# Kernel optimization log

Hardware: AMD Instinct MI355X
Metric: run time of the kernel (lower is better)

## Reference

```python
import jax, jax.numpy as jnp
import numpy as np

DIM, HEADS, KV_HEADS = 1024, 16, 4
B, T = 1, 4096
HEAD_DIM = DIM // HEADS           # 64
KV_DIM = DIM // (HEADS // KV_HEADS)  # 256
SCALE = HEAD_DIM ** -0.5


def setup_inputs() -> dict:
    key = jax.random.key(0)
    ks = jax.random.split(key, 9)
    s = lambda fan_in: fan_in ** -0.5
    return {
        "x": jax.random.normal(ks[0], (B, T, DIM), jnp.float32),
        "mask": jnp.tril(jnp.ones((1, 1, T, T), jnp.bool_)),  # causal
        "q_w": jax.random.normal(ks[1], (DIM, DIM), jnp.float32) * s(DIM),
        "q_b": jnp.zeros((DIM,), jnp.float32),
        "k_w": jax.random.normal(ks[2], (KV_DIM, DIM), jnp.float32) * s(DIM),
        "k_b": jnp.zeros((KV_DIM,), jnp.float32),
        "v_w": jax.random.normal(ks[3], (KV_DIM, DIM), jnp.float32) * s(DIM),
        "v_b": jnp.zeros((KV_DIM,), jnp.float32),
        "o_w": jax.random.normal(ks[4], (DIM, DIM), jnp.float32) * s(DIM),
        "o_b": jnp.zeros((DIM,), jnp.float32),
    }


def reference(x, mask, q_w, q_b, k_w, k_b, v_w, v_b, o_w, o_b):
    b, t, d = x.shape
    g = HEADS // KV_HEADS  # query heads per kv head
    # projections (torch Linear: x @ W^T + b)
    q = (x @ q_w.T + q_b).reshape(b, t, HEADS, HEAD_DIM).transpose(0, 2, 1, 3)      # [B,H,T,hd]
    k = (x @ k_w.T + k_b).reshape(b, t, KV_HEADS, HEAD_DIM).transpose(0, 2, 1, 3)   # [B,Hk,T,hd]
    v = (x @ v_w.T + v_b).reshape(b, t, KV_HEADS, HEAD_DIM).transpose(0, 2, 1, 3)   # [B,Hk,T,hd]
    # GQA: group query heads over shared kv heads
    qg = q.reshape(b, KV_HEADS, g, t, HEAD_DIM)                                     # [B,Hk,g,T,hd]
    scores = jnp.einsum('bkgtd,bksd->bkgts', qg, k) * SCALE                         # [B,Hk,g,T,T]
    scores = jnp.where(mask[:, :, None, :, :], scores, -1e9)
    attn = jax.nn.softmax(scores, axis=-1)  # dropout is identity in eval mode
    out = jnp.einsum('bkgts,bksd->bkgtd', attn, v)                                  # [B,Hk,g,T,hd]
    out = out.reshape(b, HEADS, t, HEAD_DIM).transpose(0, 2, 1, 3).reshape(b, t, d)
    out = out @ o_w.T + o_b
    return out, k, v  # (output, new kv cache)
```

## Files before the change

kernel.cpp:

```cpp
#include <hip/hip_runtime.h>
#include <hip/hip_bf16.h>
#include <stdint.h>

typedef __bf16 bf16;
typedef __bf16 bf16x8 __attribute__((ext_vector_type(8)));
typedef float  f32x4 __attribute__((ext_vector_type(4)));

#define SEQ   4096
#define DIM_  1024
#define HD_   64
#define NEG_BIG (-30000.0f)

__device__ __forceinline__ bf16x8 cvt8(const float* p) {
    f32x4 a = *(const f32x4*)p, b = *(const f32x4*)(p + 4);
    bf16x8 r;
    r[0]=(bf16)a[0]; r[1]=(bf16)a[1]; r[2]=(bf16)a[2]; r[3]=(bf16)a[3];
    r[4]=(bf16)b[0]; r[5]=(bf16)b[1]; r[6]=(bf16)b[2]; r[7]=(bf16)b[3];
    return r;
}

template<int MODE>
__global__ __launch_bounds__(256)
void gemm_bt(const void* __restrict__ Av,
             const float* __restrict__ B0, const float* __restrict__ b0,
             const float* __restrict__ B1, const float* __restrict__ b1,
             const float* __restrict__ B2, const float* __restrict__ b2,
             float* __restrict__ C0, float* __restrict__ C1, float* __restrict__ C2,
             bf16* __restrict__ Qbf, bf16* __restrict__ Kbf, bf16* __restrict__ VTbf)
{
    const int K = 1024;
    const int tid  = threadIdx.x;
    const int lane = tid & 63, wave = tid >> 6;
    const int qd = lane >> 4, ln = lane & 15;
    const int wm = (wave & 1) * 32, wn = (wave >> 1) * 64;
    const int m0 = blockIdx.x * 64, n0 = blockIdx.y * 128;

    const float* Bp; const float* bias;
    if (MODE == 1) {
        if (n0 < 1024)      { Bp = B0 + (size_t)n0 * K;        bias = b0 + n0; }
        else if (n0 < 1280) { Bp = B1 + (size_t)(n0-1024) * K; bias = b1 + (n0-1024); }
        else                { Bp = B2 + (size_t)(n0-1280) * K; bias = b2 + (n0-1280); }
    } else                  { Bp = B0 + (size_t)n0 * K;        bias = b0 + n0; }

    __shared__ bf16 As[64*32];
    __shared__ bf16 Bs[128*32];

    f32x4 acc[2][4] = {};

    for (int k0 = 0; k0 < K; k0 += 32) {
        bf16x8 ra, rb[2];
        {
            int row = tid >> 2, ch = tid & 3;
            if (MODE == 0)
                ra = *(const bf16x8*)((const bf16*)Av + (size_t)(m0+row)*K + k0 + ch*8);
            else
                ra = cvt8((const float*)Av + (size_t)(m0+row)*K + k0 + ch*8);
        }
        #pragma unroll
        for (int i = 0; i < 2; ++i) {
            int s = i*256 + tid;
            int row = s >> 2, ch = s & 3;
            rb[i] = cvt8(Bp + (size_t)row*K + k0 + ch*8);
        }
        __syncthreads();
        {
            int row = tid >> 2, ch = tid & 3;
            *(bf16x8*)(As + row*32 + ch*8) = ra;
        }
        #pragma unroll
        for (int i = 0; i < 2; ++i) {
            int s = i*256 + tid;
            int row = s >> 2, ch = s & 3;
            *(bf16x8*)(Bs + row*32 + ch*8) = rb[i];
        }
        __syncthreads();

        bf16x8 af[2], bg[4];
        #pragma unroll
        for (int i = 0; i < 2; ++i)
            af[i] = *(const bf16x8*)(As + (wm + i*16 + ln)*32 + qd*8);
        #pragma unroll
        for (int j = 0; j < 4; ++j)
            bg[j] = *(const bf16x8*)(Bs + (wn + j*16 + ln)*32 + qd*8);

        #pragma unroll
        for (int i = 0; i < 2; ++i)
            #pragma unroll
            for (int j = 0; j < 4; ++j)
                acc[i][j] = __builtin_amdgcn_mfma_f32_16x16x32_bf16(af[i], bg[j], acc[i][j], 0, 0, 0);
    }

    #pragma unroll
    for (int i = 0; i < 2; ++i) {
        #pragma unroll
        for (int j = 0; j < 4; ++j) {
            int colg = n0 + wn + j*16 + ln;
            float bv = bias[wn + j*16 + ln];
            #pragma unroll
            for (int r = 0; r < 4; ++r) {
                int rowg = m0 + wm + i*16 + qd*4 + r;
                float v = acc[i][j][r] + bv;
                if (MODE == 0) {
                    C0[(size_t)rowg*1024 + colg] = v;
                } else if (colg < 1024) {
                    Qbf[(size_t)rowg*1024 + colg] = (bf16)(v * 0.125f);
                } else if (colg < 1280) {
                    int c2 = colg - 1024;
                    size_t idx = (size_t)(c2 >> 6)*(SEQ*HD_) + (size_t)rowg*HD_ + (c2 & 63);
                    C1[idx]  = v;
                    Kbf[idx] = (bf16)v;
                } else {
                    int c2 = colg - 1280;
                    C2[(size_t)(c2 >> 6)*(SEQ*HD_) + (size_t)rowg*HD_ + (c2 & 63)] = v;
                    VTbf[(size_t)(c2 >> 6)*(HD_*SEQ) + (size_t)(c2 & 63)*SEQ + rowg] = (bf16)v;
                }
            }
        }
    }
}

__global__ __launch_bounds__(256)
void attn_fwd(const bf16* __restrict__ Q, const bf16* __restrict__ Kc,
              const bf16* __restrict__ VT, bf16* __restrict__ att)
{
    const int bid  = blockIdx.x;
    const int head = bid & 15;
    const int mt   = 63 - (bid >> 4);
    const int qb   = mt * 64;
    const int kvh  = head >> 2;

    const int tid = threadIdx.x, lane = tid & 63, wave = tid >> 6;
    const int qd = lane >> 4, ln = lane & 15;
    const int rw0 = qb + wave * 16;

    __shared__ bf16 Ks[64*72];
    __shared__ bf16 Vt[64*72];
    __shared__ bf16 Ps[4][16*72];

    const bf16* Kbase = Kc + (size_t)kvh * SEQ * HD_;
    const bf16* Vbase = VT + (size_t)kvh * HD_ * SEQ;

    bf16x8 aq[2];
    #pragma unroll
    for (int ks = 0; ks < 2; ++ks)
        aq[ks] = *(const bf16x8*)(Q + (size_t)(rw0 + ln)*DIM_ + head*HD_ + ks*32 + qd*8);

    f32x4 o[4] = {};
    float l_p[4] = {0.f, 0.f, 0.f, 0.f};

    const float LOG2E = 1.4426950408889634f;
    const float C16   = 16.0f * LOG2E;
    const int nkt = mt + 1;

    for (int kt = 0; kt < nkt; ++kt) {
        const int kb = kt * 64;

        bf16x8 rk[2], rv[2];
        #pragma unroll
        for (int i = 0; i < 2; ++i) {
            int s = i*256 + tid;
            int r8 = s >> 3, ch = s & 7;
            rk[i] = *(const bf16x8*)(Kbase + (size_t)(kb + r8)*HD_ + ch*8);
            rv[i] = *(const bf16x8*)(Vbase + (size_t)r8*SEQ + kb + ch*8);
        }
        __syncthreads();
        #pragma unroll
        for (int i = 0; i < 2; ++i) {
            int s = i*256 + tid;
            int r8 = s >> 3, ch = s & 7;
            *(bf16x8*)(Ks + r8*72 + ch*8) = rk[i];
            *(bf16x8*)(Vt + r8*72 + ch*8) = rv[i];
        }
        __syncthreads();

        f32x4 S[4] = {};
        #pragma unroll
        for (int ks = 0; ks < 2; ++ks) {
            bf16x8 bk[4];
            #pragma unroll
            for (int nf = 0; nf < 4; ++nf)
                bk[nf] = *(const bf16x8*)(Ks + (nf*16 + ln)*72 + ks*32 + qd*8);
            #pragma unroll
            for (int nf = 0; nf < 4; ++nf)
                S[nf] = __builtin_amdgcn_mfma_f32_16x16x32_bf16(aq[ks], bk[nf], S[nf], 0, 0, 0);
        }

        if (kt == nkt - 1) {
            #pragma unroll
            for (int nf = 0; nf < 4; ++nf) {
                int col = kb + nf*16 + ln;
                #pragma unroll
                for (int r = 0; r < 4; ++r) {
                    int row = rw0 + qd*4 + r;
                    if (col > row) S[nf][r] = NEG_BIG;
                }
            }
        }

        bf16* Pw = &Ps[wave][0];
        #pragma unroll
        for (int r = 0; r < 4; ++r) {
            #pragma unroll
            for (int nf = 0; nf < 4; ++nf) {
                float p = exp2f(S[nf][r] * LOG2E - C16);
                l_p[r] += p;
                Pw[(qd*4 + r)*72 + nf*16 + ln] = (bf16)p;
            }
        }
        asm volatile("s_waitcnt lgkmcnt(0)" ::: "memory");

        #pragma unroll
        for (int ks = 0; ks < 2; ++ks) {
            bf16x8 bv[4];
            #pragma unroll
            for (int nf = 0; nf < 4; ++nf)
                bv[nf] = *(const bf16x8*)(Vt + (nf*16 + ln)*72 + ks*32 + qd*8);
            bf16x8 ap = *(const bf16x8*)(&Ps[wave][ln*72 + ks*32 + qd*8]);
            #pragma unroll
            for (int nf = 0; nf < 4; ++nf)
                o[nf] = __builtin_amdgcn_mfma_f32_16x16x32_bf16(ap, bv[nf], o[nf], 0, 0, 0);
        }
    }

    #pragma unroll
    for (int r = 0; r < 4; ++r) {
        float l = l_p[r];
        l += __shfl_xor(l, 1);
        l += __shfl_xor(l, 2);
        l += __shfl_xor(l, 4);
        l += __shfl_xor(l, 8);
        float inv = 1.0f / l;
        int trow = rw0 + qd*4 + r;
        #pragma unroll
        for (int nf = 0; nf < 4; ++nf)
            att[(size_t)trow*DIM_ + head*HD_ + nf*16 + ln] = (bf16)(o[nf][r] * inv);
    }
}

extern "C" void kernel_launch(void* const* d_in, const int* in_sizes, int n_in,
                              void* d_out, int out_size, void* d_ws, size_t ws_size,
                              hipStream_t stream)
{
    const float* x  = (const float*)d_in[0];
    const float* qw = (const float*)d_in[2];
    const float* qb = (const float*)d_in[3];
    const float* kw = (const float*)d_in[4];
    const float* kb = (const float*)d_in[5];
    const float* vw = (const float*)d_in[6];
    const float* vb = (const float*)d_in[7];
    const float* ow = (const float*)d_in[8];
    const float* ob = (const float*)d_in[9];

    float* out  = (float*)d_out;
    float* kout = out  + (size_t)SEQ * DIM_;
    float* vout = kout + (size_t)4 * SEQ * HD_;

    bf16* q_bf  = (bf16*)d_out;
    bf16* k_bf  = q_bf + (size_t)SEQ * DIM_;
    bf16* vT_bf = k_bf + (size_t)4 * SEQ * HD_;
    bf16* att   = (bf16*)d_ws;

    gemm_bt<1><<<dim3(64, 12), 256, 0, stream>>>(x, qw, qb, kw, kb, vw, vb,
                                                 nullptr, kout, vout,
                                                 q_bf, k_bf, vT_bf);
    attn_fwd<<<dim3(1024), 256, 0, stream>>>(q_bf, k_bf, vT_bf, att);
    gemm_bt<0><<<dim3(64, 8), 256, 0, stream>>>(att, ow, ob, nullptr, nullptr,
                                                nullptr, nullptr, out, nullptr, nullptr,
                                                nullptr, nullptr, nullptr);
}
```

Before: 271.6 us.

## Pre-convert x and QKV weights to bf16 and enlarge GEMM M-tile

Adds a conversion kernel that casts x and the concatenated Q/K/V weights and biases to bf16 once, so the QKV GEMM loads bf16 directly instead of converting fp32 inside every tile. Both GEMMs move from 64x128 to 128x128 tiles with a 4x4 MFMA accumulator per wave, which raises operand reuse per shared-memory load. The cost is an extra kernel launch plus a full read and write pass for the conversion, with scratch buffers placed inside the unused part of the output buffer. The larger tiles also halve the block count and raise register use.

```diff
diff --git a/kernel.cpp b/kernel.cpp
--- a/kernel.cpp
+++ b/kernel.cpp
@@ -19,12 +19,36 @@
     return r;
 }
 
+__global__ __launch_bounds__(256)
+void cvt_pre(const float* __restrict__ x,
+             const float* __restrict__ qw, const float* __restrict__ kw,
+             const float* __restrict__ vw,
+             const float* __restrict__ qb, const float* __restrict__ kb,
+             const float* __restrict__ vb,
+             bf16* __restrict__ x_bf, bf16* __restrict__ wcat,
+             float* __restrict__ bcat)
+{
+    const int NX = (SEQ * DIM_) / 8;
+    const int NW = (1536 * 1024) / 8;
+    int i = blockIdx.x * 256 + threadIdx.x;
+    if (i < NX) {
+        *(bf16x8*)(x_bf + (size_t)i * 8) = cvt8(x + (size_t)i * 8);
+    } else if (i < NX + NW) {
+        int e = (i - NX) * 8;
+        const float* src;
+        if (e < 1024 * 1024)      src = qw + e;
+        else if (e < 1280 * 1024) src = kw + (e - 1024 * 1024);
+        else                      src = vw + (e - 1280 * 1024);
+        *(bf16x8*)(wcat + e) = cvt8(src);
+    }
+    if (i < 1536)
+        bcat[i] = (i < 1024) ? qb[i] : (i < 1280) ? kb[i - 1024] : vb[i - 1280];
+}
+
 template<int MODE>
 __global__ __launch_bounds__(256)
-void gemm_bt(const void* __restrict__ Av,
-             const float* __restrict__ B0, const float* __restrict__ b0,
-             const float* __restrict__ B1, const float* __restrict__ b1,
-             const float* __restrict__ B2, const float* __restrict__ b2,
+void gemm_bt(const bf16* __restrict__ A, const void* __restrict__ Bw,
+             const float* __restrict__ bias_all,
              float* __restrict__ C0, float* __restrict__ C1, float* __restrict__ C2,
              bf16* __restrict__ Qbf, bf16* __restrict__ Kbf, bf16* __restrict__ VTbf)
 {
@@ -32,66 +56,57 @@
     const int tid  = threadIdx.x;
     const int lane = tid & 63, wave = tid >> 6;
     const int qd = lane >> 4, ln = lane & 15;
-    const int wm = (wave & 1) * 32, wn = (wave >> 1) * 64;
-    const int m0 = blockIdx.x * 64, n0 = blockIdx.y * 128;
-
-    const float* Bp; const float* bias;
-    if (MODE == 1) {
-        if (n0 < 1024)      { Bp = B0 + (size_t)n0 * K;        bias = b0 + n0; }
-        else if (n0 < 1280) { Bp = B1 + (size_t)(n0-1024) * K; bias = b1 + (n0-1024); }
-        else                { Bp = B2 + (size_t)(n0-1280) * K; bias = b2 + (n0-1280); }
-    } else                  { Bp = B0 + (size_t)n0 * K;        bias = b0 + n0; }
-
-    __shared__ bf16 As[64*32];
+    const int wm = (wave & 1) * 64, wn = (wave >> 1) * 64;
+    const int m0 = blockIdx.x * 128, n0 = blockIdx.y * 128;
+
+    const bf16*  Bpb = (MODE == 1) ? (const bf16*)Bw + (size_t)n0 * K : nullptr;
+    const float* Bpf = (MODE == 0) ? (const float*)Bw + (size_t)n0 * K : nullptr;
+    const float* bias = bias_all + n0;
+
+    __shared__ bf16 As[128*32];
     __shared__ bf16 Bs[128*32];
 
-    f32x4 acc[2][4] = {};
+    f32x4 acc[4][4] = {};
 
     for (int k0 = 0; k0 < K; k0 += 32) {
-        bf16x8 ra, rb[2];
-        {
-            int row = tid >> 2, ch = tid & 3;
-            if (MODE == 0)
-                ra = *(const bf16x8*)((const bf16*)Av + (size_t)(m0+row)*K + k0 + ch*8);
+        bf16x8 ra[2], rb[2];
+        #pragma unroll
+        for (int i = 0; i < 2; ++i) {
+            int s   = i*256 + tid;
+            int row = s >> 2, ch = s & 3;
+            ra[i] = *(const bf16x8*)(A + (size_t)(m0+row)*K + k0 + ch*8);
+            if (MODE == 1)
+                rb[i] = *(const bf16x8*)(Bpb + (size_t)row*K + k0 + ch*8);
             else
-                ra = cvt8((const float*)Av + (size_t)(m0+row)*K + k0 + ch*8);
-        }
-        #pragma unroll
-        for (int i = 0; i < 2; ++i) {
-            int s = i*256 + tid;
+                rb[i] = cvt8(Bpf + (size_t)row*K + k0 + ch*8);
+        }
+        __syncthreads();
+        #pragma unroll
+        for (int i = 0; i < 2; ++i) {
+            int s   = i*256 + tid;
             int row = s >> 2, ch = s & 3;
-            rb[i] = cvt8(Bp + (size_t)row*K + k0 + ch*8);
-        }
-        __syncthreads();
-        {
-            int row = tid >> 2, ch = tid & 3;
-            *(bf16x8*)(As + row*32 + ch*8) = ra;
-        }
-        #pragma unroll
-        for (int i = 0; i < 2; ++i) {
-            int s = i*256 + tid;
-            int row = s >> 2, ch = s & 3;
+            *(bf16x8*)(As + row*32 + ch*8) = ra[i];
             *(bf16x8*)(Bs + row*32 + ch*8) = rb[i];
         }
         __syncthreads();
 
-        bf16x8 af[2], bg[4];
-        #pragma unroll
-        for (int i = 0; i < 2; ++i)
+        bf16x8 af[4], bg[4];
+        #pragma unroll
+        for (int i = 0; i < 4; ++i)
             af[i] = *(const bf16x8*)(As + (wm + i*16 + ln)*32 + qd*8);
         #pragma unroll
         for (int j = 0; j < 4; ++j)
             bg[j] = *(const bf16x8*)(Bs + (wn + j*16 + ln)*32 + qd*8);
 
         #pragma unroll
-        for (int i = 0; i < 2; ++i)
+        for (int i = 0; i < 4; ++i)
             #pragma unroll
             for (int j = 0; j < 4; ++j)
                 acc[i][j] = __builtin_amdgcn_mfma_f32_16x16x32_bf16(af[i], bg[j], acc[i][j], 0, 0, 0);
     }
 
     #pragma unroll
-    for (int i = 0; i < 2; ++i) {
+    for (int i = 0; i < 4; ++i) {
         #pragma unroll
         for (int j = 0; j < 4; ++j) {
             int colg = n0 + wn + j*16 + ln;
@@ -255,16 +270,21 @@
     float* kout = out  + (size_t)SEQ * DIM_;
     float* vout = kout + (size_t)4 * SEQ * HD_;
 
-    bf16* q_bf  = (bf16*)d_out;
-    bf16* k_bf  = q_bf + (size_t)SEQ * DIM_;
-    bf16* vT_bf = k_bf + (size_t)4 * SEQ * HD_;
-    bf16* att   = (bf16*)d_ws;
-
-    gemm_bt<1><<<dim3(64, 12), 256, 0, stream>>>(x, qw, qb, kw, kb, vw, vb,
+    bf16*  q_bf  = (bf16*)d_out;
+    bf16*  k_bf  = q_bf + (size_t)SEQ * DIM_;
+    bf16*  vT_bf = k_bf + (size_t)4 * SEQ * HD_;
+    bf16*  wcat  = vT_bf + (size_t)4 * HD_ * SEQ;
+    float* bcat  = (float*)(wcat + (size_t)1536*1024);
+    bf16* x_bf = (bf16*)d_ws;
+    bf16* att  = (bf16*)d_ws;
+
+    cvt_pre<<<dim3(2816), 256, 0, stream>>>(x, qw, kw, vw, qb, kb, vb,
+                                            x_bf, wcat, bcat);
+    gemm_bt<1><<<dim3(32, 12), 256, 0, stream>>>(x_bf, wcat, bcat,
                                                  nullptr, kout, vout,
                                                  q_bf, k_bf, vT_bf);
     attn_fwd<<<dim3(1024), 256, 0, stream>>>(q_bf, k_bf, vT_bf, att);
-    gemm_bt<0><<<dim3(64, 8), 256, 0, stream>>>(att, ow, ob, nullptr, nullptr,
-                                                nullptr, nullptr, out, nullptr, nullptr,
+    gemm_bt<0><<<dim3(32, 8), 256, 0, stream>>>(att, ow, ob,
+                                                out, nullptr, nullptr,
                                                 nullptr, nullptr, nullptr);
 }
```

Result: no change. 274.3 us (+1.0%).

## Enlarge GEMM tiles to 128x128 and move K/V bf16 conversion to separate kernel

Applied to the files above, without the earlier changes.

The projection GEMMs now use 128x128 output tiles, with each wave computing a 64x64 sub-tile. This doubles reuse of the converted weight tiles and halves the grid. The strided scattered bf16 stores of K and transposed V leave the GEMM epilogue. A new kv_cvt kernel does them instead, reading the fp32 K/V cache back and transposing V through shared memory so its writes are coalesced. The cost is an extra launch and an extra read of the K/V cache, plus fewer blocks per GEMM (384 and 256), which may underfill the GPU's compute units.

```diff
diff --git a/kernel.cpp b/kernel.cpp
--- a/kernel.cpp
+++ b/kernel.cpp
@@ -13,6 +13,13 @@
 
 __device__ __forceinline__ bf16x8 cvt8(const float* p) {
     f32x4 a = *(const f32x4*)p, b = *(const f32x4*)(p + 4);
+    bf16x8 r;
+    r[0]=(bf16)a[0]; r[1]=(bf16)a[1]; r[2]=(bf16)a[2]; r[3]=(bf16)a[3];
+    r[4]=(bf16)b[0]; r[5]=(bf16)b[1]; r[6]=(bf16)b[2]; r[7]=(bf16)b[3];
+    return r;
+}
+
+__device__ __forceinline__ bf16x8 pack8(f32x4 a, f32x4 b) {
     bf16x8 r;
     r[0]=(bf16)a[0]; r[1]=(bf16)a[1]; r[2]=(bf16)a[2]; r[3]=(bf16)a[3];
     r[4]=(bf16)b[0]; r[5]=(bf16)b[1]; r[6]=(bf16)b[2]; r[7]=(bf16)b[3];
@@ -26,14 +33,14 @@
              const float* __restrict__ B1, const float* __restrict__ b1,
              const float* __restrict__ B2, const float* __restrict__ b2,
              float* __restrict__ C0, float* __restrict__ C1, float* __restrict__ C2,
-             bf16* __restrict__ Qbf, bf16* __restrict__ Kbf, bf16* __restrict__ VTbf)
+             bf16* __restrict__ Qbf)
 {
     const int K = 1024;
     const int tid  = threadIdx.x;
     const int lane = tid & 63, wave = tid >> 6;
     const int qd = lane >> 4, ln = lane & 15;
-    const int wm = (wave & 1) * 32, wn = (wave >> 1) * 64;
-    const int m0 = blockIdx.x * 64, n0 = blockIdx.y * 128;
+    const int wm = (wave & 1) * 64, wn = (wave >> 1) * 64;
+    const int m0 = blockIdx.x * 128, n0 = blockIdx.y * 128;
 
     const float* Bp; const float* bias;
     if (MODE == 1) {
@@ -42,56 +49,50 @@
         else                { Bp = B2 + (size_t)(n0-1280) * K; bias = b2 + (n0-1280); }
     } else                  { Bp = B0 + (size_t)n0 * K;        bias = b0 + n0; }
 
-    __shared__ bf16 As[64*32];
+    __shared__ bf16 As[128*32];
     __shared__ bf16 Bs[128*32];
 
-    f32x4 acc[2][4] = {};
+    f32x4 acc[4][4] = {};
 
     for (int k0 = 0; k0 < K; k0 += 32) {
-        bf16x8 ra, rb[2];
-        {
-            int row = tid >> 2, ch = tid & 3;
+        bf16x8 ra[2], rb[2];
+        #pragma unroll
+        for (int i = 0; i < 2; ++i) {
+            int s   = i*256 + tid;
+            int row = s >> 2, ch = s & 3;
             if (MODE == 0)
-                ra = *(const bf16x8*)((const bf16*)Av + (size_t)(m0+row)*K + k0 + ch*8);
+                ra[i] = *(const bf16x8*)((const bf16*)Av + (size_t)(m0+row)*K + k0 + ch*8);
             else
-                ra = cvt8((const float*)Av + (size_t)(m0+row)*K + k0 + ch*8);
-        }
+                ra[i] = cvt8((const float*)Av + (size_t)(m0+row)*K + k0 + ch*8);
+            rb[i] = cvt8(Bp + (size_t)row*K + k0 + ch*8);
+        }
+        __syncthreads();
         #pragma unroll
         for (int i = 0; i < 2; ++i) {
-            int s = i*256 + tid;
+            int s   = i*256 + tid;
             int row = s >> 2, ch = s & 3;
-            rb[i] = cvt8(Bp + (size_t)row*K + k0 + ch*8);
+            *(bf16x8*)(As + row*32 + ch*8) = ra[i];
+            *(bf16x8*)(Bs + row*32 + ch*8) = rb[i];
         }
         __syncthreads();
-        {
-            int row = tid >> 2, ch = tid & 3;
-            *(bf16x8*)(As + row*32 + ch*8) = ra;
-        }
-        #pragma unroll
-        for (int i = 0; i < 2; ++i) {
-            int s = i*256 + tid;
-            int row = s >> 2, ch = s & 3;
-            *(bf16x8*)(Bs + row*32 + ch*8) = rb[i];
-        }
-        __syncthreads();
-
-        bf16x8 af[2], bg[4];
-        #pragma unroll
-        for (int i = 0; i < 2; ++i)
+
+        bf16x8 af[4], bg[4];
+        #pragma unroll
+        for (int i = 0; i < 4; ++i)
             af[i] = *(const bf16x8*)(As + (wm + i*16 + ln)*32 + qd*8);
         #pragma unroll
         for (int j = 0; j < 4; ++j)
             bg[j] = *(const bf16x8*)(Bs + (wn + j*16 + ln)*32 + qd*8);
 
         #pragma unroll
-        for (int i = 0; i < 2; ++i)
+        for (int i = 0; i < 4; ++i)
             #pragma unroll
             for (int j = 0; j < 4; ++j)
                 acc[i][j] = __builtin_amdgcn_mfma_f32_16x16x32_bf16(af[i], bg[j], acc[i][j], 0, 0, 0);
     }
 
     #pragma unroll
-    for (int i = 0; i < 2; ++i) {
+    for (int i = 0; i < 4; ++i) {
         #pragma unroll
         for (int j = 0; j < 4; ++j) {
             int colg = n0 + wn + j*16 + ln;
@@ -106,16 +107,50 @@
                     Qbf[(size_t)rowg*1024 + colg] = (bf16)(v * 0.125f);
                 } else if (colg < 1280) {
                     int c2 = colg - 1024;
-                    size_t idx = (size_t)(c2 >> 6)*(SEQ*HD_) + (size_t)rowg*HD_ + (c2 & 63);
-                    C1[idx]  = v;
-                    Kbf[idx] = (bf16)v;
+                    C1[(size_t)(c2 >> 6)*(SEQ*HD_) + (size_t)rowg*HD_ + (c2 & 63)] = v;
                 } else {
                     int c2 = colg - 1280;
                     C2[(size_t)(c2 >> 6)*(SEQ*HD_) + (size_t)rowg*HD_ + (c2 & 63)] = v;
-                    VTbf[(size_t)(c2 >> 6)*(HD_*SEQ) + (size_t)(c2 & 63)*SEQ + rowg] = (bf16)v;
                 }
             }
         }
+    }
+}
+
+__global__ __launch_bounds__(256)
+void kv_cvt(const float* __restrict__ kout, const float* __restrict__ vout,
+            bf16* __restrict__ k_bf, bf16* __restrict__ vT_bf)
+{
+    const int b   = blockIdx.x;
+    const int kvh = b >> 6, tb = b & 63;
+    const int tid = threadIdx.x;
+
+    __shared__ float T[64*65];
+
+    const float* Ksrc = kout + ((size_t)kvh*SEQ + tb*64) * HD_;
+    const float* Vsrc = vout + ((size_t)kvh*SEQ + tb*64) * HD_;
+
+    #pragma unroll
+    for (int i = 0; i < 2; ++i) {
+        int s = i*256 + tid;
+        int r = s >> 3, c = s & 7;
+        *(bf16x8*)(k_bf + ((size_t)kvh*SEQ + tb*64 + r)*HD_ + c*8)
+            = cvt8(Ksrc + (size_t)r*HD_ + c*8);
+        f32x4 va = *(const f32x4*)(Vsrc + (size_t)r*HD_ + c*8);
+        f32x4 vb = *(const f32x4*)(Vsrc + (size_t)r*HD_ + c*8 + 4);
+        #pragma unroll
+        for (int e = 0; e < 4; ++e) T[(c*8 + e)*65 + r]     = va[e];
+        #pragma unroll
+        for (int e = 0; e < 4; ++e) T[(c*8 + 4 + e)*65 + r] = vb[e];
+    }
+    __syncthreads();
+    #pragma unroll
+    for (int i = 0; i < 2; ++i) {
+        int s = i*256 + tid;
+        int d = s >> 3, c = s & 7;
+        f32x4 a = *(const f32x4*)(T + d*65 + c*8);
+        f32x4 bq = *(const f32x4*)(T + d*65 + c*8 + 4);
+        *(bf16x8*)(vT_bf + ((size_t)kvh*HD_ + d)*SEQ + tb*64 + c*8) = pack8(a, bq);
     }
 }
 
@@ -260,11 +295,11 @@
     bf16* vT_bf = k_bf + (size_t)4 * SEQ * HD_;
     bf16* att   = (bf16*)d_ws;
 
-    gemm_bt<1><<<dim3(64, 12), 256, 0, stream>>>(x, qw, qb, kw, kb, vw, vb,
-                                                 nullptr, kout, vout,
-                                                 q_bf, k_bf, vT_bf);
+    gemm_bt<1><<<dim3(32, 12), 256, 0, stream>>>(x, qw, qb, kw, kb, vw, vb,
+                                                 nullptr, kout, vout, q_bf);
+    kv_cvt<<<dim3(256), 256, 0, stream>>>(kout, vout, k_bf, vT_bf);
     attn_fwd<<<dim3(1024), 256, 0, stream>>>(q_bf, k_bf, vT_bf, att);
-    gemm_bt<0><<<dim3(64, 8), 256, 0, stream>>>(att, ow, ob, nullptr, nullptr,
+    gemm_bt<0><<<dim3(32, 8), 256, 0, stream>>>(att, ow, ob, nullptr, nullptr,
                                                 nullptr, nullptr, out, nullptr, nullptr,
-                                                nullptr, nullptr, nullptr);
-}
+                                                nullptr);
+}
```

Result: slower. 282.6 us (+4.0%).
